# Kernel tuning notes

Hardware: AMD Instinct MI355X
Metric: run time of the kernel (lower is better)

Reference implementation:

```python
import jax, jax.numpy as jnp
import numpy as np

D_MODEL = 1024
N_HEAD = 16
SEQ = 2048
BATCH = 2


def setup_inputs() -> dict:
    key = jax.random.key(0)
    x = jax.random.normal(key, (BATCH, SEQ, D_MODEL), dtype=jnp.float32)
    return {"x": x}


def reference(x) -> jnp.ndarray:
    B, S, D = x.shape
    H = N_HEAD
    hd = D // H
    # split heads: q=k=v=x -> [B, H, S, hd]
    qkv = x.reshape(B, S, H, hd).transpose(0, 2, 1, 3)
    q = k = v = qkv
    # scores [B, H, S, S], scaled by sqrt(head_dim)
    w = jnp.einsum("bhqd,bhkd->bhqk", q, k) / jnp.sqrt(jnp.asarray(hd, x.dtype))
    # causal mask (nd == ns == S here)
    causal = jnp.tril(jnp.ones((S, S), dtype=bool))
    mask_value = jnp.finfo(w.dtype).min
    w = jnp.where(causal[None, None, :, :], w, mask_value)
    w = jax.nn.softmax(w, axis=-1)
    out = jnp.einsum("bhqk,bhkd->bhqd", w, v)
    # merge heads -> [B, S, D]
    return out.transpose(0, 2, 1, 3).reshape(B, S, D)
```

## Files before the change

kernel.cpp:

```cpp
#include <hip/hip_runtime.h>

#define BATCH  2
#define SEQ    2048
#define DMODEL 1024
#define NHEAD  16
#define HD     64
#define BH     (BATCH * NHEAD)

typedef __attribute__((ext_vector_type(8))) short s8v;
typedef __attribute__((ext_vector_type(4))) float f4v;

__device__ inline unsigned short bf16_rne(float f) {
    unsigned u = __builtin_bit_cast(unsigned, f);
    u += 0x7FFFu + ((u >> 16) & 1u);
    return (unsigned short)(u >> 16);
}

__device__ __forceinline__ unsigned pk_bf16(float lo, float hi) {
    return (unsigned)bf16_rne(lo) | ((unsigned)bf16_rne(hi) << 16);
}

__global__ __launch_bounds__(256) void prep_kernel(const float* __restrict__ x,
                                                   unsigned short* __restrict__ xb,
                                                   unsigned short* __restrict__ xbT) {
    __shared__ unsigned short tile[32 * 66];
    const int id = blockIdx.x;
    const int bh = id & (BH - 1);
    const int st = id >> 5;
    const int b = bh >> 4, h = bh & (NHEAD - 1);
    const int s0 = st * 32;
    const int tid = threadIdx.x;
    const int c4 = tid & 15, r16 = tid >> 4;

#pragma unroll
    for (int p = 0; p < 2; ++p) {
        const int sl = p * 16 + r16;
        const size_t off = (size_t)(b * SEQ + s0 + sl) * DMODEL + h * HD + c4 * 4;
        float4 v = *(const float4*)(x + off);
        ushort4 o;
        o.x = bf16_rne(v.x); o.y = bf16_rne(v.y);
        o.z = bf16_rne(v.z); o.w = bf16_rne(v.w);
        *(ushort4*)(xb + off) = o;
        unsigned short* t = tile + sl * 66 + c4 * 4;
        t[0] = o.x; t[1] = o.y; t[2] = o.z; t[3] = o.w;
    }
    __syncthreads();
    {
        const int d = tid >> 2;
        const int sb = (tid & 3) * 8;
        s8v o;
#pragma unroll
        for (int j = 0; j < 8; ++j)
            o[j] = (short)tile[(sb + j) * 66 + d];
        *(s8v*)(xbT + (size_t)(bh * HD + d) * SEQ + s0 + sb) = o;
    }
}

__device__ __forceinline__ void stage_tile(const unsigned short* __restrict__ xbh,
                                           const unsigned short* __restrict__ xTh,
                                           char* lds, int bufoff, int k0,
                                           int w, int sr, int sc) {
    if (w < 2) {
#pragma unroll
        for (int i = 0; i < 4; ++i) {
            const int r = w * 32 + i * 8 + sr;
            const unsigned short* gsrc =
                xbh + (size_t)(k0 + r) * DMODEL + ((sc ^ (r & 7)) * 8);
            const int loff = __builtin_amdgcn_readfirstlane(bufoff + (w * 32 + i * 8) * 128);
            __builtin_amdgcn_global_load_lds(
                (const __attribute__((address_space(1))) void*)gsrc,
                (__attribute__((address_space(3))) void*)(lds + loff), 16, 0, 0);
        }
    } else {
#pragma unroll
        for (int i = 0; i < 4; ++i) {
            const int d = (w - 2) * 32 + i * 8 + sr;
            const unsigned short* gsrc =
                xTh + (size_t)d * SEQ + k0 + ((sc ^ (d & 7)) * 8);
            const int loff =
                __builtin_amdgcn_readfirstlane(bufoff + 8192 + ((w - 2) * 32 + i * 8) * 128);
            __builtin_amdgcn_global_load_lds(
                (const __attribute__((address_space(1))) void*)gsrc,
                (__attribute__((address_space(3))) void*)(lds + loff), 16, 0, 0);
        }
    }
}

__global__ __launch_bounds__(256, 4) void flash_kernel(const unsigned short* __restrict__ xb,
                                                       const unsigned short* __restrict__ xbT,
                                                       float* __restrict__ out,
                                                       float* __restrict__ oPart,
                                                       float* __restrict__ lPart) {
    __shared__ __align__(16) char lds[40960];

    const int id = blockIdx.x;
    const int bh = id & (BH - 1);
    const int j = id >> 5;
    int qt, kt0, ktEnd, half;
    bool partial;
    if (j < 16) {
        qt = 16 + j; kt0 = 0; ktEnd = 15; partial = true; half = 0;
    } else {
        const int r = j - 16;
        const int L = 16 - (r >> 1);
        if (r & 1) { qt = L + 15; kt0 = 16; ktEnd = qt; partial = true;  half = 1; }
        else       { qt = L - 1;  kt0 = 0;  ktEnd = qt; partial = false; half = 0; }
    }
    const int b = bh >> 4, h = bh & (NHEAD - 1);
    const int tid = threadIdx.x;
    const int w = tid >> 6;
    const int lane = tid & 63;
    const int n = lane & 15;
    const int g = lane >> 4;
    const int qbase = qt * 64;

    const unsigned short* xbh = xb + (size_t)b * SEQ * DMODEL + h * HD;
    const unsigned short* xTh = xbT + (size_t)bh * HD * SEQ;

    const int qrow = qbase + w * 16 + n;
    const s8v qf0 = *(const s8v*)(xbh + (size_t)qrow * DMODEL + g * 8);
    const s8v qf1 = *(const s8v*)(xbh + (size_t)qrow * DMODEL + 32 + g * 8);

    int roff0[4], roff1[4];
#pragma unroll
    for (int t = 0; t < 4; ++t) {
        roff0[t] = (t * 16 + n) * 128 + ((g ^ (n & 7)) * 16);
        roff1[t] = (t * 16 + n) * 128 + (((4 + g) ^ (n & 7)) * 16);
    }

    f4v o0 = {0.f, 0.f, 0.f, 0.f}, o1 = o0, o2 = o0, o3 = o0;
    float lsum = 0.0f;
    char* const Pbase = lds + 32768 + w * 2048;

    char* wrP[4];
#pragma unroll
    for (int t = 0; t < 4; ++t)
        wrP[t] = Pbase + (t >> 1) * 1024 + n * 64 +
                 ((((t & 1) * 2 + (g >> 1)) ^ (n & 3)) * 16) + (g & 1) * 8;
    const char* rdP = Pbase + n * 64 + ((g ^ (n & 3)) * 16);

    const int sr = lane >> 3;
    const int sc = lane & 7;

    stage_tile(xbh, xTh, lds, 0, kt0 * 64, w, sr, sc);

    for (int kt = kt0; kt <= ktEnd; ++kt) {
        char* const buf = lds + ((kt & 1) << 14);
        __syncthreads();
        if (kt < ktEnd)
            stage_tile(xbh, xTh, lds, ((kt & 1) ^ 1) << 14, (kt + 1) * 64, w, sr, sc);

        const bool diag = (kt == qt);
#pragma unroll
        for (int t = 0; t < 4; ++t) {
            const s8v kb0 = *(const s8v*)(buf + roff0[t]);
            const s8v kb1 = *(const s8v*)(buf + roff1[t]);
            f4v c = {0.f, 0.f, 0.f, 0.f};
            __builtin_amdgcn_s_setprio(1);
            c = __builtin_amdgcn_mfma_f32_16x16x32_bf16(kb0, qf0, c, 0, 0, 0);
            c = __builtin_amdgcn_mfma_f32_16x16x32_bf16(kb1, qf1, c, 0, 0, 0);
            __builtin_amdgcn_s_setprio(0);
            float p0, p1, p2, p3;
            {
                p0 = __builtin_amdgcn_exp2f(c[0] * 0.18033688011112042f);
                p1 = __builtin_amdgcn_exp2f(c[1] * 0.18033688011112042f);
                p2 = __builtin_amdgcn_exp2f(c[2] * 0.18033688011112042f);
                p3 = __builtin_amdgcn_exp2f(c[3] * 0.18033688011112042f);
                if (diag) {
                    const int kl = t * 16 + g * 4, ql = w * 16 + n;
                    p0 = (kl + 0 <= ql) ? p0 : 0.0f;
                    p1 = (kl + 1 <= ql) ? p1 : 0.0f;
                    p2 = (kl + 2 <= ql) ? p2 : 0.0f;
                    p3 = (kl + 3 <= ql) ? p3 : 0.0f;
                }
            }
            lsum += (p0 + p1) + (p2 + p3);
            uint2 u;
            u.x = pk_bf16(p0, p1);
            u.y = pk_bf16(p2, p3);
            *(uint2*)(wrP[t]) = u;
        }

        const s8v pa0 = *(const s8v*)(rdP);
        const s8v pa1 = *(const s8v*)(rdP + 1024);
        const char* kColB = buf + 8192;
        {
            s8v vb;
            __builtin_amdgcn_s_setprio(1);
            vb = *(const s8v*)(kColB + roff0[0]);
            o0 = __builtin_amdgcn_mfma_f32_16x16x32_bf16(pa0, vb, o0, 0, 0, 0);
            vb = *(const s8v*)(kColB + roff1[0]);
            o0 = __builtin_amdgcn_mfma_f32_16x16x32_bf16(pa1, vb, o0, 0, 0, 0);
            vb = *(const s8v*)(kColB + roff0[1]);
            o1 = __builtin_amdgcn_mfma_f32_16x16x32_bf16(pa0, vb, o1, 0, 0, 0);
            vb = *(const s8v*)(kColB + roff1[1]);
            o1 = __builtin_amdgcn_mfma_f32_16x16x32_bf16(pa1, vb, o1, 0, 0, 0);
            vb = *(const s8v*)(kColB + roff0[2]);
            o2 = __builtin_amdgcn_mfma_f32_16x16x32_bf16(pa0, vb, o2, 0, 0, 0);
            vb = *(const s8v*)(kColB + roff1[2]);
            o2 = __builtin_amdgcn_mfma_f32_16x16x32_bf16(pa1, vb, o2, 0, 0, 0);
            vb = *(const s8v*)(kColB + roff0[3]);
            o3 = __builtin_amdgcn_mfma_f32_16x16x32_bf16(pa0, vb, o3, 0, 0, 0);
            vb = *(const s8v*)(kColB + roff1[3]);
            o3 = __builtin_amdgcn_mfma_f32_16x16x32_bf16(pa1, vb, o3, 0, 0, 0);
            __builtin_amdgcn_s_setprio(0);
        }
    }

    lsum += __shfl_xor(lsum, 16, 64);
    lsum += __shfl_xor(lsum, 32, 64);

    if (!partial) {
        f4v inv;
#pragma unroll
        for (int r = 0; r < 4; ++r)
            inv[r] = 1.0f / __shfl(lsum, g * 4 + r, 64);
        float* outh = out + (size_t)b * SEQ * DMODEL + h * HD;
#pragma unroll
        for (int r = 0; r < 4; ++r) {
            const size_t rowoff = (size_t)(qbase + w * 16 + g * 4 + r) * DMODEL;
            outh[rowoff + 0 * 16 + n] = o0[r] * inv[r];
            outh[rowoff + 1 * 16 + n] = o1[r] * inv[r];
            outh[rowoff + 2 * 16 + n] = o2[r] * inv[r];
            outh[rowoff + 3 * 16 + n] = o3[r] * inv[r];
        }
    } else {
        const int slot = (bh * 16 + (qt - 16)) * 2 + half;
        float* ob = oPart + (size_t)slot * 4096;
#pragma unroll
        for (int r = 0; r < 4; ++r) {
            const int row = w * 16 + g * 4 + r;
            ob[row * 64 + 0 * 16 + n] = o0[r];
            ob[row * 64 + 1 * 16 + n] = o1[r];
            ob[row * 64 + 2 * 16 + n] = o2[r];
            ob[row * 64 + 3 * 16 + n] = o3[r];
        }
        if (g == 0) lPart[slot * 64 + w * 16 + n] = lsum;
    }
}

__global__ __launch_bounds__(256) void combine_kernel(const float* __restrict__ oPart,
                                                      const float* __restrict__ lPart,
                                                      float* __restrict__ out) {
    const int bid = blockIdx.x;
    const int bh = bid & (BH - 1);
    const int t = bid >> 5;
    const int b = bh >> 4, h = bh & (NHEAD - 1);
    const int tid = threadIdx.x;
    const int row = tid >> 2;
    const int dq = (tid & 3) * 16;
    const int slot = (bh * 16 + t) * 2;
    const float l = lPart[slot * 64 + row] + lPart[(slot + 1) * 64 + row];
    const float inv = 1.0f / l;
    const float* lo = oPart + (size_t)slot * 4096 + row * 64 + dq;
    const float* hi = lo + 4096;
    float* op = out + ((size_t)(b * SEQ + (16 + t) * 64 + row)) * DMODEL + h * HD + dq;
#pragma unroll
    for (int i = 0; i < 4; ++i) {
        float4 a = *(const float4*)(lo + i * 4);
        float4 c = *(const float4*)(hi + i * 4);
        float4 o;
        o.x = (a.x + c.x) * inv;
        o.y = (a.y + c.y) * inv;
        o.z = (a.z + c.z) * inv;
        o.w = (a.w + c.w) * inv;
        *(float4*)(op + i * 4) = o;
    }
}

#define KT 32
#define QR 16
#define LDS_STRIDE 68

__global__ __launch_bounds__(64, 2)
void attn_fp32_kernel(const float* __restrict__ x, float* __restrict__ out) {
    __shared__ float kv[KT * LDS_STRIDE];
    const int id = blockIdx.x;
    const int bh = id & (BATCH * NHEAD - 1);
    const int qt = (SEQ / QR - 1) - (id >> 5);
    const int b = bh >> 4, h = bh & (NHEAD - 1);
    const int lane = threadIdx.x;
    const int row = lane & (QR - 1);
    const int slice = lane >> 4;
    const int qrow = qt * QR + row;
    const float* xh = x + (size_t)b * SEQ * DMODEL + (size_t)h * HD;
    float q[HD], o[HD];
    const float4* qp = (const float4*)(xh + (size_t)qrow * DMODEL);
#pragma unroll
    for (int i = 0; i < HD / 4; ++i) {
        float4 v = qp[i];
        q[4*i+0] = v.x * 0.125f; q[4*i+1] = v.y * 0.125f;
        q[4*i+2] = v.z * 0.125f; q[4*i+3] = v.w * 0.125f;
    }
#pragma unroll
    for (int d = 0; d < HD; ++d) o[d] = 0.0f;
    float l = 0.0f;
    const int kend = qt * QR + QR;
    for (int kt0 = 0; kt0 < kend; kt0 += KT) {
        __syncthreads();
#pragma unroll
        for (int i = 0; i < (KT * HD / 4) / 64; ++i) {
            int idx = i * 64 + lane;
            int r = idx >> 4, c = idx & 15;
            *(float4*)(kv + r * LDS_STRIDE + c * 4) =
                *(const float4*)(xh + (size_t)(kt0 + r) * DMODEL + c * 4);
        }
        __syncthreads();
#pragma unroll 2
        for (int jj = 0; jj < KT / 4; ++jj) {
            const int j = jj * 4 + slice;
            const float* kr = kv + j * LDS_STRIDE;
            float a0 = 0.f, a1 = 0.f, a2 = 0.f, a3 = 0.f;
#pragma unroll
            for (int dq = 0; dq < 16; ++dq) {
                float4 kk = ((const float4*)kr)[dq];
                a0 = fmaf(q[4*dq+0], kk.x, a0); a1 = fmaf(q[4*dq+1], kk.y, a1);
                a2 = fmaf(q[4*dq+2], kk.z, a2); a3 = fmaf(q[4*dq+3], kk.w, a3);
            }
            float p = __expf((a0 + a1) + (a2 + a3));
            p = (kt0 + j <= qrow) ? p : 0.0f;
            l += p;
#pragma unroll
            for (int dq = 0; dq < 16; ++dq) {
                float4 vv = ((const float4*)kr)[dq];
                o[4*dq+0] = fmaf(p, vv.x, o[4*dq+0]); o[4*dq+1] = fmaf(p, vv.y, o[4*dq+1]);
                o[4*dq+2] = fmaf(p, vv.z, o[4*dq+2]); o[4*dq+3] = fmaf(p, vv.w, o[4*dq+3]);
            }
        }
    }
    l += __shfl_xor(l, 16, 64);
    l += __shfl_xor(l, 32, 64);
#pragma unroll
    for (int d = 0; d < HD; ++d) {
        o[d] += __shfl_xor(o[d], 16, 64);
        o[d] += __shfl_xor(o[d], 32, 64);
    }
    if (slice == 0) {
        const float invl = 1.0f / l;
        float4* op = (float4*)(out + ((size_t)b * SEQ + qrow) * DMODEL + (size_t)h * HD);
#pragma unroll
        for (int i = 0; i < HD / 4; ++i) {
            float4 v;
            v.x = o[4*i+0] * invl; v.y = o[4*i+1] * invl;
            v.z = o[4*i+2] * invl; v.w = o[4*i+3] * invl;
            op[i] = v;
        }
    }
}

extern "C" void kernel_launch(void* const* d_in, const int* in_sizes, int n_in,
                              void* d_out, int out_size, void* d_ws, size_t ws_size,
                              hipStream_t stream) {
    const float* x = (const float*)d_in[0];
    float* out = (float*)d_out;
    const size_t nXb = (size_t)BATCH * SEQ * DMODEL;
    const size_t nOP = (size_t)BH * 16 * 2 * 4096;
    const size_t nLP = (size_t)BH * 16 * 2 * 64;
    const size_t need = 2 * nXb * 2 + (nOP + nLP) * 4;
    if (ws_size >= need) {
        unsigned short* xb  = (unsigned short*)d_ws;
        unsigned short* xbT = xb + nXb;
        float* oPart = (float*)(xbT + nXb);
        float* lPart = oPart + nOP;
        hipLaunchKernelGGL(prep_kernel, dim3(BH * SEQ / 32), dim3(256), 0, stream,
                           x, xb, xbT);
        hipLaunchKernelGGL(flash_kernel, dim3(BH * 48), dim3(256), 0, stream,
                           xb, xbT, out, oPart, lPart);
        hipLaunchKernelGGL(combine_kernel, dim3(BH * 16), dim3(256), 0, stream,
                           oPart, lPart, out);
    } else {
        hipLaunchKernelGGL(attn_fp32_kernel, dim3(BATCH * NHEAD * (SEQ / QR)), dim3(64), 0,
                           stream, x, out);
    }
}
```

Baseline: 113.1 us.

## Process two 64-row query tiles per block to reuse K/V tiles

```diff
diff --git a/kernel.cpp b/kernel.cpp
--- a/kernel.cpp
+++ b/kernel.cpp
@@ -86,25 +86,26 @@
     }
 }
 
-__global__ __launch_bounds__(256, 4) void flash_kernel(const unsigned short* __restrict__ xb,
+__global__ __launch_bounds__(256, 3) void flash_kernel(const unsigned short* __restrict__ xb,
                                                        const unsigned short* __restrict__ xbT,
                                                        float* __restrict__ out,
                                                        float* __restrict__ oPart,
                                                        float* __restrict__ lPart) {
-    __shared__ __align__(16) char lds[40960];
+    __shared__ __align__(16) char lds[49152];
 
     const int id = blockIdx.x;
-    const int bh = id & (BH - 1);
-    const int j = id >> 5;
-    int qt, kt0, ktEnd, half;
+    const int slot = id >> 8;
+    const int c = id & 255;
+    const int bh = c & (BH - 1);
+    const int i = c >> 5;
+    int qtp, kt0, ktEnd, half;
     bool partial;
-    if (j < 16) {
-        qt = 16 + j; kt0 = 0; ktEnd = 15; partial = true; half = 0;
+    if (slot == 0) {
+        qtp = 15 - i; kt0 = 0;       ktEnd = qtp;         partial = true;  half = 0;
+    } else if (slot == 1) {
+        qtp = 15 - i; kt0 = qtp + 1; ktEnd = 2 * qtp + 1; partial = true;  half = 1;
     } else {
-        const int r = j - 16;
-        const int L = 16 - (r >> 1);
-        if (r & 1) { qt = L + 15; kt0 = 16; ktEnd = qt; partial = true;  half = 1; }
-        else       { qt = L - 1;  kt0 = 0;  ktEnd = qt; partial = false; half = 0; }
+        qtp = i;      kt0 = 0;       ktEnd = 2 * qtp + 1; partial = false; half = 0;
     }
     const int b = bh >> 4, h = bh & (NHEAD - 1);
     const int tid = threadIdx.x;
@@ -112,14 +113,17 @@
     const int lane = tid & 63;
     const int n = lane & 15;
     const int g = lane >> 4;
-    const int qbase = qt * 64;
+    const int qbase = qtp * 128;
+    const int diagA = 2 * qtp;
 
     const unsigned short* xbh = xb + (size_t)b * SEQ * DMODEL + h * HD;
     const unsigned short* xTh = xbT + (size_t)bh * HD * SEQ;
 
-    const int qrow = qbase + w * 16 + n;
-    const s8v qf0 = *(const s8v*)(xbh + (size_t)qrow * DMODEL + g * 8);
-    const s8v qf1 = *(const s8v*)(xbh + (size_t)qrow * DMODEL + 32 + g * 8);
+    const int qrowA = qbase + w * 16 + n;
+    const s8v qfA0 = *(const s8v*)(xbh + (size_t)qrowA * DMODEL + g * 8);
+    const s8v qfA1 = *(const s8v*)(xbh + (size_t)qrowA * DMODEL + 32 + g * 8);
+    const s8v qfB0 = *(const s8v*)(xbh + (size_t)(qrowA + 64) * DMODEL + g * 8);
+    const s8v qfB1 = *(const s8v*)(xbh + (size_t)(qrowA + 64) * DMODEL + 32 + g * 8);
 
     int roff0[4], roff1[4];
 #pragma unroll
@@ -128,9 +132,10 @@
         roff1[t] = (t * 16 + n) * 128 + (((4 + g) ^ (n & 7)) * 16);
     }
 
-    f4v o0 = {0.f, 0.f, 0.f, 0.f}, o1 = o0, o2 = o0, o3 = o0;
-    float lsum = 0.0f;
-    char* const Pbase = lds + 32768 + w * 2048;
+    f4v oA0 = {0.f, 0.f, 0.f, 0.f}, oA1 = oA0, oA2 = oA0, oA3 = oA0;
+    f4v oB0 = oA0, oB1 = oA0, oB2 = oA0, oB3 = oA0;
+    float lsumA = 0.0f, lsumB = 0.0f;
+    char* const Pbase = lds + 32768 + w * 4096;
 
     char* wrP[4];
 #pragma unroll
@@ -142,7 +147,7 @@
     const int sr = lane >> 3;
     const int sc = lane & 7;
 
-    stage_tile(xbh, xTh, lds, 0, kt0 * 64, w, sr, sc);
+    stage_tile(xbh, xTh, lds, (kt0 & 1) << 14, kt0 * 64, w, sr, sc);
 
     for (int kt = kt0; kt <= ktEnd; ++kt) {
         char* const buf = lds + ((kt & 1) << 14);
@@ -150,92 +155,121 @@
         if (kt < ktEnd)
             stage_tile(xbh, xTh, lds, ((kt & 1) ^ 1) << 14, (kt + 1) * 64, w, sr, sc);
 
-        const bool diag = (kt == qt);
+        const int wn = w * 16 + n;
+        const int qlA = (kt < diagA) ? 63 : ((kt == diagA) ? wn : -1);
+        const int qlB = (kt < diagA + 1) ? 63 : wn;
+
 #pragma unroll
         for (int t = 0; t < 4; ++t) {
             const s8v kb0 = *(const s8v*)(buf + roff0[t]);
             const s8v kb1 = *(const s8v*)(buf + roff1[t]);
-            f4v c = {0.f, 0.f, 0.f, 0.f};
+            f4v cA = {0.f, 0.f, 0.f, 0.f}, cB = cA;
             __builtin_amdgcn_s_setprio(1);
-            c = __builtin_amdgcn_mfma_f32_16x16x32_bf16(kb0, qf0, c, 0, 0, 0);
-            c = __builtin_amdgcn_mfma_f32_16x16x32_bf16(kb1, qf1, c, 0, 0, 0);
+            cA = __builtin_amdgcn_mfma_f32_16x16x32_bf16(kb0, qfA0, cA, 0, 0, 0);
+            cA = __builtin_amdgcn_mfma_f32_16x16x32_bf16(kb1, qfA1, cA, 0, 0, 0);
+            cB = __builtin_amdgcn_mfma_f32_16x16x32_bf16(kb0, qfB0, cB, 0, 0, 0);
+            cB = __builtin_amdgcn_mfma_f32_16x16x32_bf16(kb1, qfB1, cB, 0, 0, 0);
             __builtin_amdgcn_s_setprio(0);
-            float p0, p1, p2, p3;
-            {
-                p0 = __builtin_amdgcn_exp2f(c[0] * 0.18033688011112042f);
-                p1 = __builtin_amdgcn_exp2f(c[1] * 0.18033688011112042f);
-                p2 = __builtin_amdgcn_exp2f(c[2] * 0.18033688011112042f);
-                p3 = __builtin_amdgcn_exp2f(c[3] * 0.18033688011112042f);
-                if (diag) {
-                    const int kl = t * 16 + g * 4, ql = w * 16 + n;
-                    p0 = (kl + 0 <= ql) ? p0 : 0.0f;
-                    p1 = (kl + 1 <= ql) ? p1 : 0.0f;
-                    p2 = (kl + 2 <= ql) ? p2 : 0.0f;
-                    p3 = (kl + 3 <= ql) ? p3 : 0.0f;
-                }
+            const int kl = t * 16 + g * 4;
+            float pA[4], pB[4];
+#pragma unroll
+            for (int r = 0; r < 4; ++r) {
+                float a = __builtin_amdgcn_exp2f(cA[r] * 0.18033688011112042f);
+                float bb = __builtin_amdgcn_exp2f(cB[r] * 0.18033688011112042f);
+                pA[r] = (kl + r <= qlA) ? a : 0.0f;
+                pB[r] = (kl + r <= qlB) ? bb : 0.0f;
             }
-            lsum += (p0 + p1) + (p2 + p3);
-            uint2 u;
-            u.x = pk_bf16(p0, p1);
-            u.y = pk_bf16(p2, p3);
-            *(uint2*)(wrP[t]) = u;
-        }
-
-        const s8v pa0 = *(const s8v*)(rdP);
-        const s8v pa1 = *(const s8v*)(rdP + 1024);
+            lsumA += (pA[0] + pA[1]) + (pA[2] + pA[3]);
+            lsumB += (pB[0] + pB[1]) + (pB[2] + pB[3]);
+            uint2 uA, uB;
+            uA.x = pk_bf16(pA[0], pA[1]); uA.y = pk_bf16(pA[2], pA[3]);
+            uB.x = pk_bf16(pB[0], pB[1]); uB.y = pk_bf16(pB[2], pB[3]);
+            *(uint2*)(wrP[t]) = uA;
+            *(uint2*)(wrP[t] + 2048) = uB;
+        }
+
+        const s8v paA0 = *(const s8v*)(rdP);
+        const s8v paA1 = *(const s8v*)(rdP + 1024);
+        const s8v paB0 = *(const s8v*)(rdP + 2048);
+        const s8v paB1 = *(const s8v*)(rdP + 3072);
         const char* kColB = buf + 8192;
         {
             s8v vb;
             __builtin_amdgcn_s_setprio(1);
             vb = *(const s8v*)(kColB + roff0[0]);
-            o0 = __builtin_amdgcn_mfma_f32_16x16x32_bf16(pa0, vb, o0, 0, 0, 0);
+            oA0 = __builtin_amdgcn_mfma_f32_16x16x32_bf16(paA0, vb, oA0, 0, 0, 0);
+            oB0 = __builtin_amdgcn_mfma_f32_16x16x32_bf16(paB0, vb, oB0, 0, 0, 0);
             vb = *(const s8v*)(kColB + roff1[0]);
-            o0 = __builtin_amdgcn_mfma_f32_16x16x32_bf16(pa1, vb, o0, 0, 0, 0);
+            oA0 = __builtin_amdgcn_mfma_f32_16x16x32_bf16(paA1, vb, oA0, 0, 0, 0);
+            oB0 = __builtin_amdgcn_mfma_f32_16x16x32_bf16(paB1, vb, oB0, 0, 0, 0);
             vb = *(const s8v*)(kColB + roff0[1]);
-            o1 = __builtin_amdgcn_mfma_f32_16x16x32_bf16(pa0, vb, o1, 0, 0, 0);
+            oA1 = __builtin_amdgcn_mfma_f32_16x16x32_bf16(paA0, vb, oA1, 0, 0, 0);
+            oB1 = __builtin_amdgcn_mfma_f32_16x16x32_bf16(paB0, vb, oB1, 0, 0, 0);
             vb = *(const s8v*)(kColB + roff1[1]);
-            o1 = __builtin_amdgcn_mfma_f32_16x16x32_bf16(pa1, vb, o1, 0, 0, 0);
+            oA1 = __builtin_amdgcn_mfma_f32_16x16x32_bf16(paA1, vb, oA1, 0, 0, 0);
+            oB1 = __builtin_amdgcn_mfma_f32_16x16x32_bf16(paB1, vb, oB1, 0, 0, 0);
             vb = *(const s8v*)(kColB + roff0[2]);
-            o2 = __builtin_amdgcn_mfma_f32_16x16x32_bf16(pa0, vb, o2, 0, 0, 0);
+            oA2 = __builtin_amdgcn_mfma_f32_16x16x32_bf16(paA0, vb, oA2, 0, 0, 0);
+            oB2 = __builtin_amdgcn_mfma_f32_16x16x32_bf16(paB0, vb, oB2, 0, 0, 0);
             vb = *(const s8v*)(kColB + roff1[2]);
-            o2 = __builtin_amdgcn_mfma_f32_16x16x32_bf16(pa1, vb, o2, 0, 0, 0);
+            oA2 = __builtin_amdgcn_mfma_f32_16x16x32_bf16(paA1, vb, oA2, 0, 0, 0);
+            oB2 = __builtin_amdgcn_mfma_f32_16x16x32_bf16(paB1, vb, oB2, 0, 0, 0);
             vb = *(const s8v*)(kColB + roff0[3]);
-            o3 = __builtin_amdgcn_mfma_f32_16x16x32_bf16(pa0, vb, o3, 0, 0, 0);
+            oA3 = __builtin_amdgcn_mfma_f32_16x16x32_bf16(paA0, vb, oA3, 0, 0, 0);
+            oB3 = __builtin_amdgcn_mfma_f32_16x16x32_bf16(paB0, vb, oB3, 0, 0, 0);
             vb = *(const s8v*)(kColB + roff1[3]);
-            o3 = __builtin_amdgcn_mfma_f32_16x16x32_bf16(pa1, vb, o3, 0, 0, 0);
+            oA3 = __builtin_amdgcn_mfma_f32_16x16x32_bf16(paA1, vb, oA3, 0, 0, 0);
+            oB3 = __builtin_amdgcn_mfma_f32_16x16x32_bf16(paB1, vb, oB3, 0, 0, 0);
             __builtin_amdgcn_s_setprio(0);
         }
     }
 
-    lsum += __shfl_xor(lsum, 16, 64);
-    lsum += __shfl_xor(lsum, 32, 64);
+    lsumA += __shfl_xor(lsumA, 16, 64);
+    lsumA += __shfl_xor(lsumA, 32, 64);
+    lsumB += __shfl_xor(lsumB, 16, 64);
+    lsumB += __shfl_xor(lsumB, 32, 64);
 
     if (!partial) {
-        f4v inv;
-#pragma unroll
-        for (int r = 0; r < 4; ++r)
-            inv[r] = 1.0f / __shfl(lsum, g * 4 + r, 64);
+        f4v invA, invB;
+#pragma unroll
+        for (int r = 0; r < 4; ++r) {
+            invA[r] = 1.0f / __shfl(lsumA, g * 4 + r, 64);
+            invB[r] = 1.0f / __shfl(lsumB, g * 4 + r, 64);
+        }
         float* outh = out + (size_t)b * SEQ * DMODEL + h * HD;
 #pragma unroll
         for (int r = 0; r < 4; ++r) {
-            const size_t rowoff = (size_t)(qbase + w * 16 + g * 4 + r) * DMODEL;
-            outh[rowoff + 0 * 16 + n] = o0[r] * inv[r];
-            outh[rowoff + 1 * 16 + n] = o1[r] * inv[r];
-            outh[rowoff + 2 * 16 + n] = o2[r] * inv[r];
-            outh[rowoff + 3 * 16 + n] = o3[r] * inv[r];
+            const size_t roA = (size_t)(qbase + w * 16 + g * 4 + r) * DMODEL;
+            outh[roA + 0 * 16 + n] = oA0[r] * invA[r];
+            outh[roA + 1 * 16 + n] = oA1[r] * invA[r];
+            outh[roA + 2 * 16 + n] = oA2[r] * invA[r];
+            outh[roA + 3 * 16 + n] = oA3[r] * invA[r];
+            const size_t roB = roA + (size_t)64 * DMODEL;
+            outh[roB + 0 * 16 + n] = oB0[r] * invB[r];
+            outh[roB + 1 * 16 + n] = oB1[r] * invB[r];
+            outh[roB + 2 * 16 + n] = oB2[r] * invB[r];
+            outh[roB + 3 * 16 + n] = oB3[r] * invB[r];
         }
     } else {
-        const int slot = (bh * 16 + (qt - 16)) * 2 + half;
-        float* ob = oPart + (size_t)slot * 4096;
+        const int slotP = (bh * 8 + (qtp - 8)) * 2 + half;
+        float* ob = oPart + (size_t)slotP * 8192;
 #pragma unroll
         for (int r = 0; r < 4; ++r) {
-            const int row = w * 16 + g * 4 + r;
-            ob[row * 64 + 0 * 16 + n] = o0[r];
-            ob[row * 64 + 1 * 16 + n] = o1[r];
-            ob[row * 64 + 2 * 16 + n] = o2[r];
-            ob[row * 64 + 3 * 16 + n] = o3[r];
-        }
-        if (g == 0) lPart[slot * 64 + w * 16 + n] = lsum;
+            const int rowA = w * 16 + g * 4 + r;
+            ob[rowA * 64 + 0 * 16 + n] = oA0[r];
+            ob[rowA * 64 + 1 * 16 + n] = oA1[r];
+            ob[rowA * 64 + 2 * 16 + n] = oA2[r];
+            ob[rowA * 64 + 3 * 16 + n] = oA3[r];
+            const int rowB = rowA + 64;
+            ob[rowB * 64 + 0 * 16 + n] = oB0[r];
+            ob[rowB * 64 + 1 * 16 + n] = oB1[r];
+            ob[rowB * 64 + 2 * 16 + n] = oB2[r];
+            ob[rowB * 64 + 3 * 16 + n] = oB3[r];
+        }
+        if (g == 0) {
+            lPart[slotP * 128 + w * 16 + n] = lsumA;
+            lPart[slotP * 128 + 64 + w * 16 + n] = lsumB;
+        }
     }
 }
 
@@ -247,16 +281,16 @@
     const int t = bid >> 5;
     const int b = bh >> 4, h = bh & (NHEAD - 1);
     const int tid = threadIdx.x;
-    const int row = tid >> 2;
-    const int dq = (tid & 3) * 16;
-    const int slot = (bh * 16 + t) * 2;
-    const float l = lPart[slot * 64 + row] + lPart[(slot + 1) * 64 + row];
+    const int row = tid >> 1;
+    const int dq = (tid & 1) * 32;
+    const int slotP = (bh * 8 + t) * 2;
+    const float l = lPart[slotP * 128 + row] + lPart[(slotP + 1) * 128 + row];
     const float inv = 1.0f / l;
-    const float* lo = oPart + (size_t)slot * 4096 + row * 64 + dq;
-    const float* hi = lo + 4096;
-    float* op = out + ((size_t)(b * SEQ + (16 + t) * 64 + row)) * DMODEL + h * HD + dq;
-#pragma unroll
-    for (int i = 0; i < 4; ++i) {
+    const float* lo = oPart + (size_t)slotP * 8192 + row * 64 + dq;
+    const float* hi = lo + 8192;
+    float* op = out + ((size_t)(b * SEQ + (8 + t) * 128 + row)) * DMODEL + h * HD + dq;
+#pragma unroll
+    for (int i = 0; i < 8; ++i) {
         float4 a = *(const float4*)(lo + i * 4);
         float4 c = *(const float4*)(hi + i * 4);
         float4 o;
@@ -301,9 +335,9 @@
 #pragma unroll
         for (int i = 0; i < (KT * HD / 4) / 64; ++i) {
             int idx = i * 64 + lane;
-            int r = idx >> 4, c = idx & 15;
-            *(float4*)(kv + r * LDS_STRIDE + c * 4) =
-                *(const float4*)(xh + (size_t)(kt0 + r) * DMODEL + c * 4);
+            int r = idx >> 4, cc = idx & 15;
+            *(float4*)(kv + r * LDS_STRIDE + cc * 4) =
+                *(const float4*)(xh + (size_t)(kt0 + r) * DMODEL + cc * 4);
         }
         __syncthreads();
 #pragma unroll 2
@@ -354,8 +388,8 @@
     const float* x = (const float*)d_in[0];
     float* out = (float*)d_out;
     const size_t nXb = (size_t)BATCH * SEQ * DMODEL;
-    const size_t nOP = (size_t)BH * 16 * 2 * 4096;
-    const size_t nLP = (size_t)BH * 16 * 2 * 64;
+    const size_t nOP = (size_t)BH * 8 * 2 * 8192;
+    const size_t nLP = (size_t)BH * 8 * 2 * 128;
     const size_t need = 2 * nXb * 2 + (nOP + nLP) * 4;
     if (ws_size >= need) {
         unsigned short* xb  = (unsigned short*)d_ws;
@@ -364,9 +398,9 @@
         float* lPart = oPart + nOP;
         hipLaunchKernelGGL(prep_kernel, dim3(BH * SEQ / 32), dim3(256), 0, stream,
                            x, xb, xbT);
-        hipLaunchKernelGGL(flash_kernel, dim3(BH * 48), dim3(256), 0, stream,
+        hipLaunchKernelGGL(flash_kernel, dim3(768), dim3(256), 0, stream,
                            xb, xbT, out, oPart, lPart);
-        hipLaunchKernelGGL(combine_kernel, dim3(BH * 16), dim3(256), 0, stream,
+        hipLaunchKernelGGL(combine_kernel, dim3(BH * 8), dim3(256), 0, stream,
                            oPart, lPart, out);
     } else {
         hipLaunchKernelGGL(attn_fp32_kernel, dim3(BATCH * NHEAD * (SEQ / QR)), dim3(64), 0,
```

Result: no change. 114.0 us (+0.8%).
